# Kernel tuning notes

Hardware: AMD Instinct MI355X
Metric: run time of the kernel (lower is better)

The kernel has to match this reference:

```python
import jax, jax.numpy as jnp
import numpy as np

K_F = 3          # propagation kernel
PAD_F = 1
NUM = K_F * K_F - 1   # 8 non-reference neighbors
IDX_REF = NUM // 2    # 4
PROP_TIME = 18
B, H, W = 4, 240, 1216


def _conv2d_same(x, w, b):
    # x: (B,Cin,H,W), w: (Cout,Cin,kh,kw)
    y = jax.lax.conv_general_dilated(x, w, (1, 1), 'SAME',
                                     dimension_numbers=('NCHW', 'OIHW', 'NCHW'))
    return y + b[None, :, None, None]


def _bilinear(img, y, x):
    # img: (B,H,W); y,x: (B,K,H,W) float sample coords. Zero outside bounds (DCN semantics).
    Bv, Hv, Wv = img.shape
    flat = img.reshape(Bv, -1)
    y0 = jnp.floor(y)
    x0 = jnp.floor(x)
    wy = y - y0
    wx = x - x0

    def g(yy, xx):
        valid = (yy >= 0) & (yy <= Hv - 1) & (xx >= 0) & (xx <= Wv - 1)
        yc = jnp.clip(yy, 0, Hv - 1).astype(jnp.int32)
        xc = jnp.clip(xx, 0, Wv - 1).astype(jnp.int32)
        idx = (yc * Wv + xc).reshape(Bv, -1)
        v = jnp.take_along_axis(flat, idx, axis=1).reshape(yy.shape)
        return jnp.where(valid, v, jnp.zeros((), img.dtype))

    return ((1 - wy) * (1 - wx) * g(y0, x0)
            + (1 - wy) * wx * g(y0, x0 + 1)
            + wy * (1 - wx) * g(y1 := y0 + 1, x0)
            + wy * wx * g(y1, x0 + 1))


def _deform_agg(feat, off, mask, k, pad):
    # Modulated deformable conv with w == 1, b == 0, ch_f == 1.
    # feat: (B,1,H,W); off: (B,K,2,H,W) (dy,dx); mask: (B,K,H,W)
    Bv, _, Hv, Wv = feat.shape
    kk = jnp.arange(k)
    by = (jnp.repeat(kk, k) - pad).astype(feat.dtype)  # kernel base dy, row-major
    bx = (jnp.tile(kk, k) - pad).astype(feat.dtype)    # kernel base dx
    gy = jnp.arange(Hv, dtype=feat.dtype)[None, None, :, None]
    gx = jnp.arange(Wv, dtype=feat.dtype)[None, None, None, :]
    y = gy + by[None, :, None, None] + off[:, :, 0]
    x = gx + bx[None, :, None, None] + off[:, :, 1]
    s = _bilinear(feat[:, 0], y, x)                    # (B,K,H,W)
    return jnp.sum(s * mask, axis=1, keepdims=True)


def setup_inputs() -> dict:
    key = jax.random.key(0)
    k1, k2, k3, k4, k5, k6 = jax.random.split(key, 6)
    feat_init = jax.random.uniform(k1, (B, 1, H, W), jnp.float32)
    guidance = jax.random.normal(k2, (B, 8, H, W), jnp.float32)
    confidence = jax.random.uniform(k3, (B, 1, H, W), jnp.float32)
    dep = jax.random.uniform(k4, (B, 1, H, W), jnp.float32)
    valid = (jax.random.uniform(k5, (B, 1, H, W), jnp.float32) < 0.05)
    feat_fix = dep * valid.astype(jnp.float32)
    w_oa = 0.1 * jax.random.normal(k6, (3 * NUM, 8, 3, 3), jnp.float32)
    b_oa = jnp.zeros((3 * NUM,), jnp.float32)
    aff_scale_const = jnp.full((1,), 0.5 * NUM, jnp.float32)  # gamma * num (TGASS)
    return {'feat_init': feat_init, 'guidance': guidance, 'confidence': confidence,
            'feat_fix': feat_fix, 'w_oa': w_oa, 'b_oa': b_oa,
            'aff_scale_const': aff_scale_const}


def reference(feat_init, guidance, confidence, feat_fix, w_oa, b_oa, aff_scale_const):
    Bv, _, Hv, Wv = guidance.shape
    oa = _conv2d_same(guidance, w_oa, b_oa)                 # (B,24,H,W)
    o1, o2, aff = oa[:, :NUM], oa[:, NUM:2 * NUM], oa[:, 2 * NUM:]
    # torch: cat((o1,o2),1).view(B,num,2,H,W) then insert zero ref offset at idx_ref
    off = jnp.concatenate([o1, o2], axis=1).reshape(Bv, NUM, 2, Hv, Wv)
    zeros = jnp.zeros((Bv, 1, 2, Hv, Wv), off.dtype)
    off = jnp.concatenate([off[:, :IDX_REF], zeros, off[:, IDX_REF:]], axis=1)  # (B,9,2,H,W)

    # TGASS affinity
    aff = jnp.tanh(aff) / (aff_scale_const + 1e-8)          # (B,8,H,W)

    # confidence-weighted affinity: 1x1 deform-sample of confidence at each neighbor offset
    nbr = jnp.array([0, 1, 2, 3, 5, 6, 7, 8])
    off_c = jax.lax.stop_gradient(off[:, nbr])              # (B,8,2,H,W), offsets detached
    gy = jnp.arange(Hv, dtype=aff.dtype)[None, None, :, None]
    gx = jnp.arange(Wv, dtype=aff.dtype)[None, None, None, :]
    conf_aff = _bilinear(confidence[:, 0], gy + off_c[:, :, 0], gx + off_c[:, :, 1])
    aff = aff * conf_aff

    s = jnp.sum(jnp.abs(aff), axis=1, keepdims=True) + 1e-4
    s = jnp.maximum(s, 1.0)                                 # TGASS clamp
    aff = aff / s
    aff_ref = 1.0 - jnp.sum(aff, axis=1, keepdims=True)
    aff9 = jnp.concatenate([aff[:, :IDX_REF], aff_ref, aff[:, IDX_REF:]], axis=1)  # (B,9,H,W)

    # preserve_input mask
    mask_fix = (jnp.sum((feat_fix > 0.0).astype(feat_fix.dtype), axis=1, keepdims=True) > 0.0)
    mask_fix = jax.lax.stop_gradient(mask_fix.astype(feat_fix.dtype))

    def step(feat, _):
        feat = (1.0 - mask_fix) * feat + mask_fix * feat_fix
        feat = _deform_agg(feat, off, aff9, K_F, PAD_F)
        return feat, None

    feat_result, _ = jax.lax.scan(step, feat_init, None, length=PROP_TIME)
    return feat_result, off.reshape(Bv, -1, Hv, Wv), aff9
```

## Files before the change

kernel.cpp:

```cpp
#include <hip/hip_runtime.h>
#include <hip/hip_bf16.h>
#include <hip/hip_cooperative_groups.h>

namespace cg = cooperative_groups;

#define B_ 4
#define H_ 240
#define W_ 1216
#define HW_ (H_*W_)
#define N1_ (B_*HW_)
#define PT_ 18

#define PR_ 4
#define TROWS2 (PR_ + 10)
#define TCOLS 274

__device__ __forceinline__ bool probe_bf16(const void* scale_ptr) {
    return ((const unsigned short*)scale_ptr)[0] == 0x4080;
}

__device__ __forceinline__ float ldin(const void* p, int i, bool bf) {
    if (bf) {
        unsigned int u = (unsigned int)((const unsigned short*)p)[i];
        return __uint_as_float(u << 16);
    }
    return ((const float*)p)[i];
}

__device__ __forceinline__ void stout(void* p, int i, bool bf, float v) {
    if (bf) ((__hip_bfloat16*)p)[i] = __float2bfloat16(v);
    else    ((float*)p)[i] = v;
}

template<bool BF>
__device__ __forceinline__ float ldT(const void* p, int i) {
    if (BF) {
        unsigned int u = (unsigned int)((const unsigned short*)p)[i];
        return __uint_as_float(u << 16);
    }
    return ((const float*)p)[i];
}

template<bool BF>
__device__ __forceinline__ void stT(void* p, int i, float v) {
    if (BF) ((__hip_bfloat16*)p)[i] = __float2bfloat16(v);
    else    ((float*)p)[i] = v;
}

__global__ __launch_bounds__(256) void k_prep_w(const void* __restrict__ w_oa,
                                                const void* __restrict__ b_oa,
                                                const void* __restrict__ scale,
                                                float* __restrict__ wc) {
    bool bf = probe_bf16(scale);
    int i = blockIdx.x * 256 + threadIdx.x;
    if (i < 1728) wc[i] = ldin(w_oa, i, bf);
    if (i < 24)   wc[1728 + i] = ldin(b_oa, i, bf);
}

__global__ __launch_bounds__(256) void k_init(const void* __restrict__ finit,
                                              const void* __restrict__ ffix,
                                              const void* __restrict__ scale,
                                              float* __restrict__ featA,
                                              float* __restrict__ featB,
                                              unsigned long long* __restrict__ mask64) {
    bool bf = probe_bf16(scale);
    int p = blockIdx.x * 256 + threadIdx.x;
    float fx = ldin(ffix, p, bf);
    float fi = ldin(finit, p, bf);
    bool fixed = fx > 0.0f;
    float v = fixed ? fx : fi;
    featA[p] = v;
    featB[p] = v;
    unsigned long long bal = __ballot(fixed);
    if ((threadIdx.x & 63) == 0) mask64[p >> 6] = bal;
}

__global__ __launch_bounds__(256) void k_conv(const void* __restrict__ guid,
                                              const void* __restrict__ conf,
                                              const void* __restrict__ scale,
                                              const float* __restrict__ wc,
                                              void* __restrict__ d_out,
                                              float* __restrict__ ws_off,
                                              float* __restrict__ ws_aff,
                                              int mode2) {
    bool bf = probe_bf16(scale);
    int p = blockIdx.x * 256 + threadIdx.x;
    if (p >= N1_) return;
    int b = p / HW_;
    int r = p - b * HW_;
    int h = r / W_;
    int w = r - h * W_;

    float g[8][9];
    #pragma unroll
    for (int t = 0; t < 9; ++t) {
        int hh = h + t / 3 - 1;
        int ww = w + t % 3 - 1;
        bool v = (hh >= 0) && (hh < H_) && (ww >= 0) && (ww < W_);
        int idx0 = hh * W_ + ww;
        #pragma unroll
        for (int ci = 0; ci < 8; ++ci)
            g[ci][t] = v ? ldin(guid, (b * 8 + ci) * HW_ + idx0, bf) : 0.0f;
    }

    float oa[24];
    #pragma unroll
    for (int co = 0; co < 24; ++co) {
        float a = wc[1728 + co];
        #pragma unroll
        for (int ci = 0; ci < 8; ++ci)
            #pragma unroll
            for (int t = 0; t < 9; ++t)
                a = fmaf(g[ci][t], wc[(co * 8 + ci) * 9 + t], a);
        oa[co] = a;
    }

    float scl = ldin(scale, 0, bf);
    float inv = 1.0f / (scl + 1e-8f);

    float aft[8];
    int cbase = b * HW_;
    #pragma unroll
    for (int t = 0; t < 8; ++t) {
        float a = tanhf(oa[16 + t]) * inv;
        float y = (float)h + oa[2 * t];
        float x = (float)w + oa[2 * t + 1];
        float y0f = floorf(y), x0f = floorf(x);
        int y0 = (int)y0f, x0 = (int)x0f;
        float wy = y - y0f, wx = x - x0f;
        int y0c = min(max(y0, 0), H_ - 1), y1c = min(max(y0 + 1, 0), H_ - 1);
        int x0c = min(max(x0, 0), W_ - 1), x1c = min(max(x0 + 1, 0), W_ - 1);
        bool vy0 = (y0 >= 0) && (y0 < H_), vy1 = (y0 >= -1) && (y0 < H_ - 1);
        bool vx0 = (x0 >= 0) && (x0 < W_), vx1 = (x0 >= -1) && (x0 < W_ - 1);
        float w00 = (1.0f - wy) * (1.0f - wx); w00 = (vy0 && vx0) ? w00 : 0.0f;
        float w01 = (1.0f - wy) * wx;          w01 = (vy0 && vx1) ? w01 : 0.0f;
        float w10 = wy * (1.0f - wx);          w10 = (vy1 && vx0) ? w10 : 0.0f;
        float w11 = wy * wx;                   w11 = (vy1 && vx1) ? w11 : 0.0f;
        float f00 = ldin(conf, cbase + y0c * W_ + x0c, bf);
        float f01 = ldin(conf, cbase + y0c * W_ + x1c, bf);
        float f10 = ldin(conf, cbase + y1c * W_ + x0c, bf);
        float f11 = ldin(conf, cbase + y1c * W_ + x1c, bf);
        float cv = w00 * f00 + w01 * f01 + w10 * f10 + w11 * f11;
        aft[t] = a * cv;
    }
    float s = 1e-4f;
    #pragma unroll
    for (int t = 0; t < 8; ++t) s += fabsf(aft[t]);
    s = fmaxf(s, 1.0f);
    float rs = 1.0f / s;
    float suma = 0.0f;
    #pragma unroll
    for (int t = 0; t < 8; ++t) { aft[t] *= rs; suma += aft[t]; }
    float aref = 1.0f - suma;

    #pragma unroll
    for (int t = 0; t < 8; ++t) {
        int n9 = t + (t >= 4 ? 1 : 0);
        stout(d_out, N1_ + (b * 18 + 2 * n9)     * HW_ + r, bf, oa[2 * t]);
        stout(d_out, N1_ + (b * 18 + 2 * n9 + 1) * HW_ + r, bf, oa[2 * t + 1]);
        stout(d_out, 19 * N1_ + (b * 9 + n9) * HW_ + r, bf, aft[t]);
    }
    stout(d_out, N1_ + (b * 18 + 8) * HW_ + r, bf, 0.0f);
    stout(d_out, N1_ + (b * 18 + 9) * HW_ + r, bf, 0.0f);
    stout(d_out, 19 * N1_ + (b * 9 + 4) * HW_ + r, bf, aref);

    if (mode2 && bf) {
        #pragma unroll
        for (int t = 0; t < 8; ++t) {
            ws_off[t * N1_ + p]       = oa[2 * t];
            ws_off[(8 + t) * N1_ + p] = oa[2 * t + 1];
            int n9 = t + (t >= 4 ? 1 : 0);
            ws_aff[n9 * N1_ + p] = aft[t];
        }
        ws_aff[4 * N1_ + p] = aref;
    }
}

template<bool BF>
__device__ __forceinline__ float prop_px(const float (*tile)[TCOLS],
                                         const float* __restrict__ sp,
                                         const float* oy, const float* ox,
                                         const float* af,
                                         int h, int w, int ry,
                                         int row0, int col0, int tx) {
    float acc = af[4] * tile[5 + ry][tx + 8];
    #pragma unroll
    for (int t = 0; t < 8; ++t) {
        int n9 = t + (t >= 4 ? 1 : 0);
        float y = (float)(h + n9 / 3 - 1) + oy[t];
        float x = (float)(w + n9 % 3 - 1) + ox[t];
        float y0f = floorf(y), x0f = floorf(x);
        int y0 = (int)y0f, x0 = (int)x0f;
        float wy = y - y0f, wx = x - x0f;
        int y0c = min(max(y0, 0), H_ - 1), y1c = min(max(y0 + 1, 0), H_ - 1);
        int x0c = min(max(x0, 0), W_ - 1), x1c = min(max(x0 + 1, 0), W_ - 1);
        bool vy0 = (y0 >= 0) && (y0 < H_), vy1 = (y0 >= -1) && (y0 < H_ - 1);
        bool vx0 = (x0 >= 0) && (x0 < W_), vx1 = (x0 >= -1) && (x0 < W_ - 1);
        float w00 = (1.0f - wy) * (1.0f - wx); w00 = (vy0 && vx0) ? w00 : 0.0f;
        float w01 = (1.0f - wy) * wx;          w01 = (vy0 && vx1) ? w01 : 0.0f;
        float w10 = wy * (1.0f - wx);          w10 = (vy1 && vx0) ? w10 : 0.0f;
        float w11 = wy * wx;                   w11 = (vy1 && vx1) ? w11 : 0.0f;
        int sy0 = y0c - row0, sy1 = y1c - row0;
        int sx0 = x0c - col0, sx1 = x1c - col0;
        float f00, f01, f10, f11;
        if ((sy0 >= 0) && (sy1 <= TROWS2 - 1) && (sx0 >= 0) && (sx1 <= TCOLS - 1)) {
            f00 = tile[sy0][sx0];
            f01 = tile[sy0][sx1];
            f10 = tile[sy1][sx0];
            f11 = tile[sy1][sx1];
        } else {
            f00 = sp[y0c * W_ + x0c];
            f01 = sp[y0c * W_ + x1c];
            f10 = sp[y1c * W_ + x0c];
            f11 = sp[y1c * W_ + x1c];
        }
        float v = w00 * f00 + w01 * f01 + w10 * f10 + w11 * f11;
        acc = fmaf(af[n9], v, acc);
    }
    return acc;
}

template<bool BF>
__device__ __forceinline__ void load_meta(float* oy, float* ox, float* af,
                                          const float* __restrict__ ws_off,
                                          const float* __restrict__ ws_aff,
                                          const void* __restrict__ d_out_all,
                                          bool use_ws, int b, int r, int p) {
    if (use_ws) {
        #pragma unroll
        for (int t = 0; t < 8; ++t) {
            oy[t] = ws_off[t * N1_ + p];
            ox[t] = ws_off[(8 + t) * N1_ + p];
        }
        #pragma unroll
        for (int n = 0; n < 9; ++n) af[n] = ws_aff[n * N1_ + p];
    } else {
        #pragma unroll
        for (int t = 0; t < 8; ++t) {
            int n9 = t + (t >= 4 ? 1 : 0);
            oy[t] = ldT<BF>(d_out_all, N1_ + (b * 18 + 2 * n9)     * HW_ + r);
            ox[t] = ldT<BF>(d_out_all, N1_ + (b * 18 + 2 * n9 + 1) * HW_ + r);
        }
        #pragma unroll
        for (int n = 0; n < 9; ++n)
            af[n] = ldT<BF>(d_out_all, 19 * N1_ + (b * 9 + n) * HW_ + r);
    }
}

template<bool BF>
__device__ __forceinline__ void fused_body(float (*tile)[TCOLS],
                                           float* __restrict__ bufA,
                                           float* __restrict__ bufB,
                                           const float* __restrict__ ws_off,
                                           const float* __restrict__ ws_aff,
                                           const void* __restrict__ d_out_all,
                                           const unsigned long long* __restrict__ mask64,
                                           void* __restrict__ d_out_feat,
                                           int mode2) {
    cg::grid_group grid = cg::this_grid();
    int tx = threadIdx.x;
    int bx = blockIdx.x;
    int h0 = blockIdx.y * PR_;
    int b  = blockIdx.z;
    int w  = bx * 256 + tx;
    bool active = (w < W_);
    bool use_ws = BF && (mode2 != 0);
    int row0 = h0 - 5;
    int col0 = bx * 256 - 8;

    float oy[PR_][8], ox[PR_][8], af[PR_][9];
    if (active) {
        #pragma unroll
        for (int ry = 0; ry < PR_; ++ry) {
            int r = (h0 + ry) * W_ + w;
            int p = b * HW_ + r;
            load_meta<BF>(oy[ry], ox[ry], af[ry], ws_off, ws_aff, d_out_all,
                          use_ws, b, r, p);
        }
    }

    const float* src = bufA;
    float* dst = bufB;
    for (int it = 0; it < PT_; ++it) {
        const float* sp = src + b * HW_;
        for (int idx = tx; idx < TROWS2 * TCOLS; idx += 256) {
            int rr = idx / TCOLS;
            int cc = idx - rr * TCOLS;
            int gy = min(max(row0 + rr, 0), H_ - 1);
            int gx = min(max(col0 + cc, 0), W_ - 1);
            tile[rr][cc] = sp[gy * W_ + gx];
        }
        __syncthreads();

        if (active) {
            #pragma unroll
            for (int ry = 0; ry < PR_; ++ry) {
                int h = h0 + ry;
                int r = h * W_ + w;
                int p = b * HW_ + r;
                float acc = prop_px<BF>(tile, sp, oy[ry], ox[ry], af[ry],
                                        h, w, ry, row0, col0, tx);
                if (it == PT_ - 1) {
                    stT<BF>(d_out_feat, p, acc);
                } else {
                    unsigned long long bal = mask64[p >> 6];
                    bool fixed = (bal >> (p & 63)) & 1ull;
                    if (!fixed) dst[p] = acc;
                }
            }
        }

        if (it < PT_ - 1) {
            const float* t = src; src = dst; dst = (float*)t;
            grid.sync();
        }
    }
}

__global__ __launch_bounds__(256) void k_prop_fused(float* bufA, float* bufB,
                                                    const float* ws_off,
                                                    const float* ws_aff,
                                                    const void* d_out_all,
                                                    const unsigned long long* mask64,
                                                    const void* scale,
                                                    void* d_out_feat,
                                                    int mode2) {
    __shared__ float tile[TROWS2][TCOLS];
    if (probe_bf16(scale))
        fused_body<true>(tile, bufA, bufB, ws_off, ws_aff, d_out_all, mask64,
                         d_out_feat, mode2);
    else
        fused_body<false>(tile, bufA, bufB, ws_off, ws_aff, d_out_all, mask64,
                          d_out_feat, mode2);
}

template<bool BF>
__device__ __forceinline__ void prop_body(float (*tile)[TCOLS],
                                          const float* __restrict__ src,
                                          float* __restrict__ dst,
                                          const float* __restrict__ ws_off,
                                          const float* __restrict__ ws_aff,
                                          const void* __restrict__ d_out_all,
                                          const unsigned long long* __restrict__ mask64,
                                          void* __restrict__ d_out_feat,
                                          int last, int mode2) {
    int tx = threadIdx.x;
    int bx = blockIdx.x;
    int h0 = blockIdx.y * PR_;
    int b  = blockIdx.z;
    int w  = bx * 256 + tx;
    bool active = (w < W_);
    bool use_ws = BF && (mode2 != 0);
    const float* sp = src + b * HW_;
    int row0 = h0 - 5;
    int col0 = bx * 256 - 8;

    for (int idx = tx; idx < TROWS2 * TCOLS; idx += 256) {
        int rr = idx / TCOLS;
        int cc = idx - rr * TCOLS;
        int gy = min(max(row0 + rr, 0), H_ - 1);
        int gx = min(max(col0 + cc, 0), W_ - 1);
        tile[rr][cc] = sp[gy * W_ + gx];
    }
    __syncthreads();
    if (!active) return;

    for (int ry = 0; ry < PR_; ++ry) {
        int h = h0 + ry;
        int r = h * W_ + w;
        int p = b * HW_ + r;
        float oy[8], ox[8], af[9];
        load_meta<BF>(oy, ox, af, ws_off, ws_aff, d_out_all, use_ws, b, r, p);
        float acc = prop_px<BF>(tile, sp, oy, ox, af, h, w, ry, row0, col0, tx);
        if (last) {
            stT<BF>(d_out_feat, p, acc);
        } else {
            unsigned long long bal = mask64[p >> 6];
            bool fixed = (bal >> (p & 63)) & 1ull;
            if (!fixed) dst[p] = acc;
        }
    }
}

__global__ __launch_bounds__(256) void k_prop(const float* __restrict__ src,
                                              float* __restrict__ dst,
                                              const float* __restrict__ ws_off,
                                              const float* __restrict__ ws_aff,
                                              const void* __restrict__ d_out_all,
                                              const unsigned long long* __restrict__ mask64,
                                              const void* __restrict__ scale,
                                              void* __restrict__ d_out_feat,
                                              int last, int mode2) {
    __shared__ float tile[TROWS2][TCOLS];
    if (probe_bf16(scale))
        prop_body<true>(tile, src, dst, ws_off, ws_aff, d_out_all, mask64,
                        d_out_feat, last, mode2);
    else
        prop_body<false>(tile, src, dst, ws_off, ws_aff, d_out_all, mask64,
                         d_out_feat, last, mode2);
}

extern "C" void kernel_launch(void* const* d_in, const int* in_sizes, int n_in,
                              void* d_out, int out_size, void* d_ws, size_t ws_size,
                              hipStream_t stream) {
    const void* feat_init  = d_in[0];
    const void* guidance   = d_in[1];
    const void* confidence = d_in[2];
    const void* feat_fix   = d_in[3];
    const void* w_oa       = d_in[4];
    const void* b_oa       = d_in[5];
    const void* scale      = d_in[6];

    float* wsf    = (float*)d_ws;
    float* featA  = wsf;
    float* featB  = wsf + N1_;
    float* wc     = wsf + 2 * (size_t)N1_;
    unsigned long long* mask64 =
        (unsigned long long*)(wsf + 2 * (size_t)N1_ + 2048);
    float* ws_off = wsf + 2 * (size_t)N1_ + 2048 + 36480;
    float* ws_aff = ws_off + 16 * (size_t)N1_;

    size_t need2 = ((size_t)27 * N1_ + 2048 + 36480) * sizeof(float);
    int mode2 = (ws_size >= need2) ? 1 : 0;

    int grid = N1_ / 256;
    hipLaunchKernelGGL(k_prep_w, dim3(7), dim3(256), 0, stream, w_oa, b_oa, scale, wc);
    hipLaunchKernelGGL(k_init, dim3(grid), dim3(256), 0, stream,
                       feat_init, feat_fix, scale, featA, featB, mask64);
    hipLaunchKernelGGL(k_conv, dim3(grid), dim3(256), 0, stream,
                       guidance, confidence, scale, wc, d_out, ws_off, ws_aff, mode2);

    dim3 pgrid(5, H_ / PR_, B_);
    bool fused_ok = false;
    int maxBlocksPerCU = 0;
    hipError_t qe = hipOccupancyMaxActiveBlocksPerMultiprocessor(
        &maxBlocksPerCU, (const void*)k_prop_fused, 256, 0);
    if (qe == hipSuccess && maxBlocksPerCU * 256 >= (int)(5 * (H_ / PR_) * B_)) {
        void* args[] = { (void*)&featA, (void*)&featB,
                         (void*)&ws_off, (void*)&ws_aff,
                         (void*)&d_out, (void*)&mask64,
                         (void*)&scale, (void*)&d_out, (void*)&mode2 };
        hipError_t le = hipLaunchCooperativeKernel(
            (const void*)k_prop_fused, pgrid, dim3(256), args, 0, stream);
        fused_ok = (le == hipSuccess);
    }

    if (!fused_ok) {
        float* a = featA;
        float* bbuf = featB;
        for (int it = 0; it < PT_; ++it) {
            int last = (it == PT_ - 1) ? 1 : 0;
            hipLaunchKernelGGL(k_prop, pgrid, dim3(256), 0, stream,
                               a, bbuf, ws_off, ws_aff, d_out, mask64, scale,
                               d_out, last, mode2);
            float* t = a; a = bbuf; bbuf = t;
        }
    }
}
```

Before: 946.2 us.

## Reload propagation metadata per iteration in cooperative kernel and enlarge row tile

Result: no change. 938.0 us (-0.9%).

```diff
diff --git a/kernel.cpp b/kernel.cpp
--- a/kernel.cpp
+++ b/kernel.cpp
@@ -13,6 +13,8 @@
 
 #define PR_ 4
 #define TROWS2 (PR_ + 10)
+#define PRF_ 5
+#define TROWSF (PRF_ + 10)
 #define TCOLS 274
 
 __device__ __forceinline__ bool probe_bf16(const void* scale_ptr) {
@@ -176,7 +178,7 @@
     }
 }
 
-template<bool BF>
+template<bool BF, int TR>
 __device__ __forceinline__ float prop_px(const float (*tile)[TCOLS],
                                          const float* __restrict__ sp,
                                          const float* oy, const float* ox,
@@ -203,7 +205,7 @@
         int sy0 = y0c - row0, sy1 = y1c - row0;
         int sx0 = x0c - col0, sx1 = x1c - col0;
         float f00, f01, f10, f11;
-        if ((sy0 >= 0) && (sy1 <= TROWS2 - 1) && (sx0 >= 0) && (sx1 <= TCOLS - 1)) {
+        if ((sy0 >= 0) && (sy1 <= TR - 1) && (sx0 >= 0) && (sx1 <= TCOLS - 1)) {
             f00 = tile[sy0][sx0];
             f01 = tile[sy0][sx1];
             f10 = tile[sy1][sx0];
@@ -241,9 +243,20 @@
             oy[t] = ldT<BF>(d_out_all, N1_ + (b * 18 + 2 * n9)     * HW_ + r);
             ox[t] = ldT<BF>(d_out_all, N1_ + (b * 18 + 2 * n9 + 1) * HW_ + r);
         }
-        #pragma unroll
-        for (int n = 0; n < 9; ++n)
-            af[n] = ldT<BF>(d_out_all, 19 * N1_ + (b * 9 + n) * HW_ + r);
+        if (BF) {
+            #pragma unroll
+            for (int n = 0; n < 9; ++n)
+                af[n] = ldT<BF>(d_out_all, 19 * N1_ + (b * 9 + n) * HW_ + r);
+        } else {
+            #pragma unroll
+            for (int t = 0; t < 8; ++t) {
+                int n9 = t + (t >= 4 ? 1 : 0);
+                af[n9] = ldT<BF>(d_out_all, 19 * N1_ + (b * 9 + n9) * HW_ + r);
+            }
+            float suma = af[0]; suma += af[1]; suma += af[2]; suma += af[3];
+            suma += af[5]; suma += af[6]; suma += af[7]; suma += af[8];
+            af[4] = 1.0f - suma;
+        }
     }
 }
 
@@ -260,7 +273,7 @@
     cg::grid_group grid = cg::this_grid();
     int tx = threadIdx.x;
     int bx = blockIdx.x;
-    int h0 = blockIdx.y * PR_;
+    int h0 = blockIdx.y * PRF_;
     int b  = blockIdx.z;
     int w  = bx * 256 + tx;
     bool active = (w < W_);
@@ -268,22 +281,11 @@
     int row0 = h0 - 5;
     int col0 = bx * 256 - 8;
 
-    float oy[PR_][8], ox[PR_][8], af[PR_][9];
-    if (active) {
-        #pragma unroll
-        for (int ry = 0; ry < PR_; ++ry) {
-            int r = (h0 + ry) * W_ + w;
-            int p = b * HW_ + r;
-            load_meta<BF>(oy[ry], ox[ry], af[ry], ws_off, ws_aff, d_out_all,
-                          use_ws, b, r, p);
-        }
-    }
-
     const float* src = bufA;
     float* dst = bufB;
     for (int it = 0; it < PT_; ++it) {
         const float* sp = src + b * HW_;
-        for (int idx = tx; idx < TROWS2 * TCOLS; idx += 256) {
+        for (int idx = tx; idx < TROWSF * TCOLS; idx += 256) {
             int rr = idx / TCOLS;
             int cc = idx - rr * TCOLS;
             int gy = min(max(row0 + rr, 0), H_ - 1);
@@ -294,12 +296,15 @@
 
         if (active) {
             #pragma unroll
-            for (int ry = 0; ry < PR_; ++ry) {
+            for (int ry = 0; ry < PRF_; ++ry) {
                 int h = h0 + ry;
                 int r = h * W_ + w;
                 int p = b * HW_ + r;
-                float acc = prop_px<BF>(tile, sp, oy[ry], ox[ry], af[ry],
-                                        h, w, ry, row0, col0, tx);
+                float oy[8], ox[8], af[9];
+                load_meta<BF>(oy, ox, af, ws_off, ws_aff, d_out_all,
+                              use_ws, b, r, p);
+                float acc = prop_px<BF, TROWSF>(tile, sp, oy, ox, af,
+                                                h, w, ry, row0, col0, tx);
                 if (it == PT_ - 1) {
                     stT<BF>(d_out_feat, p, acc);
                 } else {
@@ -314,18 +319,19 @@
             const float* t = src; src = dst; dst = (float*)t;
             grid.sync();
         }
-    }
-}
-
-__global__ __launch_bounds__(256) void k_prop_fused(float* bufA, float* bufB,
-                                                    const float* ws_off,
-                                                    const float* ws_aff,
-                                                    const void* d_out_all,
-                                                    const unsigned long long* mask64,
-                                                    const void* scale,
-                                                    void* d_out_feat,
-                                                    int mode2) {
-    __shared__ float tile[TROWS2][TCOLS];
+        __syncthreads();
+    }
+}
+
+__global__ __launch_bounds__(256, 4) void k_prop_fused(float* bufA, float* bufB,
+                                                       const float* ws_off,
+                                                       const float* ws_aff,
+                                                       const void* d_out_all,
+                                                       const unsigned long long* mask64,
+                                                       const void* scale,
+                                                       void* d_out_feat,
+                                                       int mode2) {
+    __shared__ float tile[TROWSF][TCOLS];
     if (probe_bf16(scale))
         fused_body<true>(tile, bufA, bufB, ws_off, ws_aff, d_out_all, mask64,
                          d_out_feat, mode2);
@@ -371,7 +377,8 @@
         int p = b * HW_ + r;
         float oy[8], ox[8], af[9];
         load_meta<BF>(oy, ox, af, ws_off, ws_aff, d_out_all, use_ws, b, r, p);
-        float acc = prop_px<BF>(tile, sp, oy, ox, af, h, w, ry, row0, col0, tx);
+        float acc = prop_px<BF, TROWS2>(tile, sp, oy, ox, af,
+                                        h, w, ry, row0, col0, tx);
         if (last) {
             stT<BF>(d_out_feat, p, acc);
         } else {
@@ -430,22 +437,23 @@
     hipLaunchKernelGGL(k_conv, dim3(grid), dim3(256), 0, stream,
                        guidance, confidence, scale, wc, d_out, ws_off, ws_aff, mode2);
 
-    dim3 pgrid(5, H_ / PR_, B_);
+    dim3 fgrid(5, H_ / PRF_, B_);
     bool fused_ok = false;
     int maxBlocksPerCU = 0;
     hipError_t qe = hipOccupancyMaxActiveBlocksPerMultiprocessor(
         &maxBlocksPerCU, (const void*)k_prop_fused, 256, 0);
-    if (qe == hipSuccess && maxBlocksPerCU * 256 >= (int)(5 * (H_ / PR_) * B_)) {
+    if (qe == hipSuccess && maxBlocksPerCU * 256 >= (int)(5 * (H_ / PRF_) * B_)) {
         void* args[] = { (void*)&featA, (void*)&featB,
                          (void*)&ws_off, (void*)&ws_aff,
                          (void*)&d_out, (void*)&mask64,
                          (void*)&scale, (void*)&d_out, (void*)&mode2 };
         hipError_t le = hipLaunchCooperativeKernel(
-            (const void*)k_prop_fused, pgrid, dim3(256), args, 0, stream);
+            (const void*)k_prop_fused, fgrid, dim3(256), args, 0, stream);
         fused_ok = (le == hipSuccess);
     }
 
     if (!fused_ok) {
+        dim3 pgrid(5, H_ / PR_, B_);
         float* a = featA;
         float* bbuf = featB;
         for (int it = 0; it < PT_; ++it) {
```
